# Kernel tuning notes

Measured on AMD Instinct MI355X. Metric: run time of the kernel, lower is better.

Reference implementation:

```python
import jax, jax.numpy as jnp
import numpy as np
import math

B, T, D = 2, 2048, 1024
N_EXP, TOP_K = 8, 2
CAP_FACTOR = 1.25  # train_capacity (module in training mode)
MIN_CAP = 4


def _capacity(num_tokens):
    cap = math.floor(TOP_K * CAP_FACTOR * num_tokens / N_EXP)
    cap += cap % 2
    return max(cap, MIN_CAP)


def setup_inputs() -> dict:
    key = jax.random.key(0)
    k1, k2 = jax.random.split(key)
    x = jax.random.normal(k1, (B, T, D), dtype=jnp.float32)
    w_g = jax.random.normal(k2, (N_EXP, D), dtype=jnp.float32) * 0.02
    return {"x": x, "w_g": w_g}


def reference(x, w_g):
    Bx, Tx, Dx = x.shape
    n_tok = Bx * Tx
    cap = _capacity(n_tok)  # static: depends only on shapes

    # router runs in full precision (router_use_full_prec=True)
    logits = jnp.einsum('btd,ed->bte', x.astype(jnp.float32), w_g.astype(jnp.float32))
    logits = logits.reshape(n_tok, N_EXP)

    top_v, top_i = jax.lax.top_k(logits, TOP_K)          # [n_tok, k]
    # softmax over (-inf)-masked logits == softmax over the k selected logits
    probs_k = jax.nn.softmax(top_v, axis=-1)             # [n_tok, k]

    # expert one-hot mask, ordered [k, tokens, n_exp] (matches torch permute)
    exp_mask = jax.nn.one_hot(top_i, N_EXP, dtype=jnp.int32)   # [n_tok, k, n_exp]
    exp_mask = jnp.transpose(exp_mask, (1, 0, 2))              # [k, n_tok, n_exp]

    # position-in-expert-queue rank via cumsum over flattened (k*tokens)
    rank = jnp.cumsum(exp_mask.reshape(TOP_K * n_tok, N_EXP), axis=0) - 1
    rank = rank.reshape(TOP_K, n_tok, N_EXP)

    exp_mask = exp_mask * (rank < cap).astype(jnp.int32)       # drop overflow tokens
    used_capacity = jnp.sum(exp_mask, axis=(0, 1))             # [n_exp]

    rank_sel = jnp.sum(exp_mask * rank, axis=-1)               # [k, n_tok] int
    keep = jnp.sum(exp_mask, axis=-1).astype(jnp.float32)      # [k, n_tok] 0/1
    w_sel = probs_k.T * keep                                   # [k, n_tok]

    # combine weights: scatter instead of the O(k*tok*n_exp*cap) outer product
    cb_weight = jnp.zeros((n_tok, N_EXP, cap), dtype=jnp.float32)
    tok_ids = jnp.arange(n_tok)
    for k in range(TOP_K):  # tiny static loop over top_k
        cb_weight = cb_weight.at[tok_ids, top_i[:, k], rank_sel[k]].add(w_sel[k])

    sec_mask = cb_weight != 0
    return used_capacity, cb_weight, sec_mask
```

## Files before the change

kernel.cpp:

```cpp
#include <hip/hip_runtime.h>

#define N_TOK   4096
#define DDIM    1024
#define N_EXP   8
#define CAP     1280
#define ROW     (N_EXP * CAP)
#define CB_ELEMS (N_TOK * ROW)

typedef __attribute__((ext_vector_type(4))) float f32x4;


__global__ __launch_bounds__(256) void router_kernel(
    const float* __restrict__ x, const float* __restrict__ wg,
    unsigned int* __restrict__ pk,
    float* __restrict__ p0, float* __restrict__ p1)
{
    __shared__ int se0[4], se1[4];
    const int wave = threadIdx.x >> 6;
    const int lane = threadIdx.x & 63;
    const int t = blockIdx.x * 4 + wave;

    const float4* xt  = (const float4*)(x + (size_t)t * DDIM);
    const float4* wg4 = (const float4*)wg;

    float acc[N_EXP];
#pragma unroll
    for (int e = 0; e < N_EXP; ++e) acc[e] = 0.f;

#pragma unroll
    for (int it = 0; it < 4; ++it) {
        const int d4 = lane + it * 64;
        const float4 xv = xt[d4];
#pragma unroll
        for (int e = 0; e < N_EXP; ++e) {
            const float4 wv = wg4[e * 256 + d4];
            acc[e] = fmaf(xv.x, wv.x,
                     fmaf(xv.y, wv.y,
                     fmaf(xv.z, wv.z,
                     fmaf(xv.w, wv.w, acc[e]))));
        }
    }

#pragma unroll
    for (int e = 0; e < N_EXP; ++e) {
#pragma unroll
        for (int off = 32; off >= 1; off >>= 1)
            acc[e] += __shfl_xor(acc[e], off, 64);
    }

    if (lane == 0) {
        float v0 = -3.402823466e38f, v1 = -3.402823466e38f;
        int   i0 = 0, i1 = 0;
#pragma unroll
        for (int e = 0; e < N_EXP; ++e) {
            const float v = acc[e];
            if (v > v0)      { v1 = v0; i1 = i0; v0 = v; i0 = e; }
            else if (v > v1) { v1 = v;  i1 = e; }
        }
        const float ex  = expf(v1 - v0);
        const float inv = 1.f / (1.f + ex);
        p0[t] = inv;
        p1[t] = ex * inv;
        se0[wave] = i0;
        se1[wave] = i1;
    }
    __syncthreads();

    if (threadIdx.x == 0) {
        const int b = blockIdx.x;
        unsigned short* pks = (unsigned short*)pk;
        const unsigned short h0 = (unsigned short)(se0[0] | (se0[1] << 4) |
                                                   (se0[2] << 8) | (se0[3] << 12));
        const unsigned short h1 = (unsigned short)(se1[0] | (se1[1] << 4) |
                                                   (se1[2] << 8) | (se1[3] << 12));
        pks[b]        = h0;
        pks[1024 + b] = h1;
    }
}

__global__ __launch_bounds__(256) void fill_kernel(
    const unsigned int* __restrict__ pk, const float* __restrict__ p0,
    const float* __restrict__ p1, float* __restrict__ out)
{
    __shared__ int s_e[4], s_r[4];

    const int  b     = blockIdx.x;
    const bool is_cb = (b < 2048);
    const int  t0    = (is_cb ? b : (b - 2048)) * 2;

    const int wave = threadIdx.x >> 6;
    const int lane = threadIdx.x & 63;
    const int tt   = t0 + (wave >> 1);
    const int i    = (wave & 1) * N_TOK + tt;

    unsigned int w[16];
#pragma unroll
    for (int j = 0; j < 16; ++j) w[j] = pk[lane + j * 64];
    const unsigned int wi = pk[i >> 3];

    float* base = out + 8 + (is_cb ? 0 : (size_t)CB_ELEMS) + (size_t)t0 * ROW;
    f32x4* b4   = (f32x4*)base;
    const f32x4 z = {0.f, 0.f, 0.f, 0.f};
#pragma unroll
    for (int it = 0; it < 20; ++it)
        b4[threadIdx.x + it * 256] = z;

    const int e = (int)((wi >> ((i & 7) * 4)) & 0xF);
    int cnt = 0;
#pragma unroll
    for (int j = 0; j < 16; ++j) {
        const int bi = (lane + j * 64) * 8;
#pragma unroll
        for (int s = 0; s < 8; ++s)
            cnt += (bi + s < i && (int)((w[j] >> (4 * s)) & 0xF) == e) ? 1 : 0;
    }
#pragma unroll
    for (int off = 32; off >= 1; off >>= 1)
        cnt += __shfl_xor(cnt, off, 64);
    if (lane == 0) { s_e[wave] = e; s_r[wave] = cnt; }

    __syncthreads();

    if (threadIdx.x < 4) {
        const int r = s_r[threadIdx.x];
        if (r < CAP) {
            const int   t2 = t0 + (threadIdx.x >> 1);
            const float wv = (threadIdx.x & 1) ? p1[t2] : p0[t2];
            const float v  = is_cb ? wv : ((wv != 0.f) ? 1.f : 0.f);
            base[(size_t)(t2 - t0) * ROW + s_e[threadIdx.x] * CAP + r] = v;
        }
    }

    if (b == 0) {
#pragma unroll
        for (int q = 0; q < 2; ++q) {
            const int ee = wave * 2 + q;
            int c = 0;
#pragma unroll
            for (int j = 0; j < 16; ++j) {
#pragma unroll
                for (int s = 0; s < 8; ++s)
                    c += ((int)((w[j] >> (4 * s)) & 0xF) == ee) ? 1 : 0;
            }
#pragma unroll
            for (int off = 32; off >= 1; off >>= 1)
                c += __shfl_xor(c, off, 64);
            if (lane == 0) out[ee] = (float)min(c, CAP);
        }
    }
}

extern "C" void kernel_launch(void* const* d_in, const int* in_sizes, int n_in,
                              void* d_out, int out_size, void* d_ws, size_t ws_size,
                              hipStream_t stream)
{
    const float* x  = (const float*)d_in[0];
    const float* wg = (const float*)d_in[1];
    float* out = (float*)d_out;

    char*         ws = (char*)d_ws;
    unsigned int* pk = (unsigned int*)(ws);
    float*        p0 = (float*)(ws + 4096);
    float*        p1 = (float*)(ws + 20480);

    router_kernel<<<N_TOK / 4, 256, 0, stream>>>(x, wg, pk, p0, p1);
    fill_kernel<<<4096, 256, 0, stream>>>(pk, p0, p1, out);
}
```

Measured before the change: 78.20 us.

## Process sixteen tokens per 1024-thread fill block with packed expert ids staged in LDS

Restructures the fill kernel from 4096 blocks of 256 threads, each handling two tokens, to 512 blocks of 1024 threads, each handling sixteen tokens. The packed top-k expert table is loaded once into shared memory and every wave reads it from there instead of from global memory. One wave now computes the ranks for both top-k slots of its token. The aim is to cut per-block overhead and redundant global reads of the expert table. Each block now zeroes a larger contiguous chunk, which reduces the block count and could lower memory-level parallelism or tail balance.

```diff
diff --git a/kernel.cpp b/kernel.cpp
--- a/kernel.cpp
+++ b/kernel.cpp
@@ -6,6 +6,13 @@
 #define CAP     1280
 #define ROW     (N_EXP * CAP)
 #define CB_ELEMS (N_TOK * ROW)
+
+#define FBLK        512
+#define FTHR        1024
+#define CHUNK_F32   163840
+#define CHUNK4      (CHUNK_F32 / 4)
+#define FITERS      (CHUNK4 / FTHR)
+#define TOK_PER_BLK 16
 
 typedef __attribute__((ext_vector_type(4))) float f32x4;
 
@@ -78,74 +85,77 @@
     }
 }
 
-__global__ __launch_bounds__(256) void fill_kernel(
+__global__ __launch_bounds__(1024) void fill_kernel(
     const unsigned int* __restrict__ pk, const float* __restrict__ p0,
     const float* __restrict__ p1, float* __restrict__ out)
 {
-    __shared__ int s_e[4], s_r[4];
+    __shared__ unsigned int spk[1024];
+    __shared__ int s_e[32], s_r[32];
 
     const int  b     = blockIdx.x;
-    const bool is_cb = (b < 2048);
-    const int  t0    = (is_cb ? b : (b - 2048)) * 2;
+    const bool is_cb = (b < FBLK / 2);
+    const int  tbase = (is_cb ? b : (b - FBLK / 2)) * TOK_PER_BLK;
+
+    spk[threadIdx.x] = pk[threadIdx.x];
+    __syncthreads();
+
+    float* base = out + 8 + (size_t)b * CHUNK_F32;
+    f32x4* b4   = (f32x4*)base;
+    const f32x4 z = {0.f, 0.f, 0.f, 0.f};
+#pragma unroll
+    for (int it = 0; it < FITERS; ++it)
+        b4[threadIdx.x + it * FTHR] = z;
 
     const int wave = threadIdx.x >> 6;
     const int lane = threadIdx.x & 63;
-    const int tt   = t0 + (wave >> 1);
-    const int i    = (wave & 1) * N_TOK + tt;
+    const int tt   = tbase + wave;
 
     unsigned int w[16];
 #pragma unroll
-    for (int j = 0; j < 16; ++j) w[j] = pk[lane + j * 64];
-    const unsigned int wi = pk[i >> 3];
+    for (int j = 0; j < 16; ++j) w[j] = spk[lane + j * 64];
 
-    float* base = out + 8 + (is_cb ? 0 : (size_t)CB_ELEMS) + (size_t)t0 * ROW;
-    f32x4* b4   = (f32x4*)base;
-    const f32x4 z = {0.f, 0.f, 0.f, 0.f};
 #pragma unroll
-    for (int it = 0; it < 20; ++it)
-        b4[threadIdx.x + it * 256] = z;
+    for (int k = 0; k < 2; ++k) {
+        const int i = k * N_TOK + tt;
+        const int e = (int)((spk[i >> 3] >> ((i & 7) * 4)) & 0xF);
+        int cnt = 0;
+#pragma unroll
+        for (int j = 0; j < 16; ++j) {
+            const int bi = (lane + j * 64) * 8;
+#pragma unroll
+            for (int s = 0; s < 8; ++s)
+                cnt += (bi + s < i && (int)((w[j] >> (4 * s)) & 0xF) == e) ? 1 : 0;
+        }
+#pragma unroll
+        for (int off = 32; off >= 1; off >>= 1)
+            cnt += __shfl_xor(cnt, off, 64);
+        if (lane == 0) { s_e[wave * 2 + k] = e; s_r[wave * 2 + k] = cnt; }
+    }
 
-    const int e = (int)((wi >> ((i & 7) * 4)) & 0xF);
-    int cnt = 0;
+    if (b == 0 && wave < N_EXP) {
+        int c = 0;
 #pragma unroll
-    for (int j = 0; j < 16; ++j) {
-        const int bi = (lane + j * 64) * 8;
+        for (int j = 0; j < 16; ++j) {
 #pragma unroll
-        for (int s = 0; s < 8; ++s)
-            cnt += (bi + s < i && (int)((w[j] >> (4 * s)) & 0xF) == e) ? 1 : 0;
+            for (int s = 0; s < 8; ++s)
+                c += ((int)((w[j] >> (4 * s)) & 0xF) == wave) ? 1 : 0;
+        }
+#pragma unroll
+        for (int off = 32; off >= 1; off >>= 1)
+            c += __shfl_xor(c, off, 64);
+        if (lane == 0) out[wave] = (float)min(c, CAP);
     }
-#pragma unroll
-    for (int off = 32; off >= 1; off >>= 1)
-        cnt += __shfl_xor(cnt, off, 64);
-    if (lane == 0) { s_e[wave] = e; s_r[wave] = cnt; }
 
     __syncthreads();
 
-    if (threadIdx.x < 4) {
+    if (threadIdx.x < 32) {
         const int r = s_r[threadIdx.x];
         if (r < CAP) {
-            const int   t2 = t0 + (threadIdx.x >> 1);
+            const int   t2 = tbase + (threadIdx.x >> 1);
             const float wv = (threadIdx.x & 1) ? p1[t2] : p0[t2];
             const float v  = is_cb ? wv : ((wv != 0.f) ? 1.f : 0.f);
-            base[(size_t)(t2 - t0) * ROW + s_e[threadIdx.x] * CAP + r] = v;
-        }
-    }
-
-    if (b == 0) {
-#pragma unroll
-        for (int q = 0; q < 2; ++q) {
-            const int ee = wave * 2 + q;
-            int c = 0;
-#pragma unroll
-            for (int j = 0; j < 16; ++j) {
-#pragma unroll
-                for (int s = 0; s < 8; ++s)
-                    c += ((int)((w[j] >> (4 * s)) & 0xF) == ee) ? 1 : 0;
-            }
-#pragma unroll
-            for (int off = 32; off >= 1; off >>= 1)
-                c += __shfl_xor(c, off, 64);
-            if (lane == 0) out[ee] = (float)min(c, CAP);
+            base[(size_t)(threadIdx.x >> 1) * ROW
+                 + (size_t)s_e[threadIdx.x] * CAP + r] = v;
         }
     }
 }
@@ -164,5 +174,5 @@
     float*        p1 = (float*)(ws + 20480);
 
     router_kernel<<<N_TOK / 4, 256, 0, stream>>>(x, wg, pk, p0, p1);
-    fill_kernel<<<4096, 256, 0, stream>>>(pk, p0, p1, out);
+    fill_kernel<<<FBLK, FTHR, 0, stream>>>(pk, p0, p1, out);
 }
```

After: 219.7 us. +181.0%, slower.

## Align fill blocks to 16B chunks and stage packed expert ids in LDS

Applied to the files above, without the earlier changes.

Each fill block now zeroes a contiguous, 16-byte-aligned chunk of the output, replacing the per-token rows that were offset by the 8-element used_capacity header. This keeps the f32x4 zero stores aligned. Each block computes ranks for the tokens whose nonzero entries can land in its chunk, including neighbouring and edge tokens, and writes a value only if it falls inside its own range. The packed expert ids are first staged in shared memory. In exchange, each block does about twice the rank-counting work and the boundary bookkeeping becomes more complex.

```diff
diff --git a/kernel.cpp b/kernel.cpp
--- a/kernel.cpp
+++ b/kernel.cpp
@@ -6,6 +6,7 @@
 #define CAP     1280
 #define ROW     (N_EXP * CAP)
 #define CB_ELEMS (N_TOK * ROW)
+#define CHUNK   20480
 
 typedef __attribute__((ext_vector_type(4))) float f32x4;
 
@@ -82,72 +83,101 @@
     const unsigned int* __restrict__ pk, const float* __restrict__ p0,
     const float* __restrict__ p1, float* __restrict__ out)
 {
-    __shared__ int s_e[4], s_r[4];
+    __shared__ unsigned int spk[1024];
+    __shared__ int s_e[8], s_r[8], s_used[8];
 
-    const int  b     = blockIdx.x;
-    const bool is_cb = (b < 2048);
-    const int  t0    = (is_cb ? b : (b - 2048)) * 2;
+    const int b  = blockIdx.x;
+    const int lo = b * CHUNK;
 
-    const int wave = threadIdx.x >> 6;
-    const int lane = threadIdx.x & 63;
-    const int tt   = t0 + (wave >> 1);
-    const int i    = (wave & 1) * N_TOK + tt;
-
-    unsigned int w[16];
-#pragma unroll
-    for (int j = 0; j < 16; ++j) w[j] = pk[lane + j * 64];
-    const unsigned int wi = pk[i >> 3];
-
-    float* base = out + 8 + (is_cb ? 0 : (size_t)CB_ELEMS) + (size_t)t0 * ROW;
-    f32x4* b4   = (f32x4*)base;
+    f32x4* b4 = (f32x4*)out + (size_t)b * (CHUNK / 4);
     const f32x4 z = {0.f, 0.f, 0.f, 0.f};
 #pragma unroll
     for (int it = 0; it < 20; ++it)
         b4[threadIdx.x + it * 256] = z;
+    if (b == 4095 && threadIdx.x < 2)
+        ((f32x4*)out)[(size_t)4096 * (CHUNK / 4) + threadIdx.x] = z;
 
-    const int e = (int)((wi >> ((i & 7) * 4)) & 0xF);
-    int cnt = 0;
 #pragma unroll
-    for (int j = 0; j < 16; ++j) {
-        const int bi = (lane + j * 64) * 8;
-#pragma unroll
-        for (int s = 0; s < 8; ++s)
-            cnt += (bi + s < i && (int)((w[j] >> (4 * s)) & 0xF) == e) ? 1 : 0;
-    }
-#pragma unroll
-    for (int off = 32; off >= 1; off >>= 1)
-        cnt += __shfl_xor(cnt, off, 64);
-    if (lane == 0) { s_e[wave] = e; s_r[wave] = cnt; }
-
+    for (int j = 0; j < 4; ++j)
+        spk[threadIdx.x + j * 256] = pk[threadIdx.x + j * 256];
     __syncthreads();
 
-    if (threadIdx.x < 4) {
-        const int r = s_r[threadIdx.x];
-        if (r < CAP) {
-            const int   t2 = t0 + (threadIdx.x >> 1);
-            const float wv = (threadIdx.x & 1) ? p1[t2] : p0[t2];
-            const float v  = is_cb ? wv : ((wv != 0.f) ? 1.f : 0.f);
-            base[(size_t)(t2 - t0) * ROW + s_e[threadIdx.x] * CAP + r] = v;
+    const int wave = threadIdx.x >> 6;
+    const int lane = threadIdx.x & 63;
+    const int c    = b & 2047;
+    const int t0   = 2 * c;
+    const int tc   = (wave == 0) ? t0 - 1 : (wave == 1) ? t0 :
+                     (wave == 2) ? t0 + 1 : ((b == 2048) ? N_TOK - 1 : -1);
+
+    unsigned int w[16];
+#pragma unroll
+    for (int j = 0; j < 16; ++j) w[j] = spk[lane + j * 64];
+
+    if (tc >= 0 && tc < N_TOK) {
+#pragma unroll
+        for (int k = 0; k < 2; ++k) {
+            const int i = k * N_TOK + tc;
+            const int e = (int)((spk[i >> 3] >> ((i & 7) * 4)) & 0xF);
+            int cnt = 0;
+#pragma unroll
+            for (int j = 0; j < 16; ++j) {
+                const int bi = (lane + j * 64) * 8;
+#pragma unroll
+                for (int s = 0; s < 8; ++s)
+                    cnt += (bi + s < i &&
+                            (int)((w[j] >> (4 * s)) & 0xF) == e) ? 1 : 0;
+            }
+#pragma unroll
+            for (int off = 32; off >= 1; off >>= 1)
+                cnt += __shfl_xor(cnt, off, 64);
+            if (lane == 0) { s_e[wave * 2 + k] = e; s_r[wave * 2 + k] = cnt; }
         }
+    } else if (lane == 0) {
+        s_r[wave * 2] = 1 << 20; s_r[wave * 2 + 1] = 1 << 20;
+        s_e[wave * 2] = 0;       s_e[wave * 2 + 1] = 0;
     }
 
     if (b == 0) {
 #pragma unroll
         for (int q = 0; q < 2; ++q) {
             const int ee = wave * 2 + q;
-            int c = 0;
+            int cu = 0;
 #pragma unroll
             for (int j = 0; j < 16; ++j) {
 #pragma unroll
                 for (int s = 0; s < 8; ++s)
-                    c += ((int)((w[j] >> (4 * s)) & 0xF) == ee) ? 1 : 0;
+                    cu += ((int)((w[j] >> (4 * s)) & 0xF) == ee) ? 1 : 0;
             }
 #pragma unroll
             for (int off = 32; off >= 1; off >>= 1)
-                c += __shfl_xor(c, off, 64);
-            if (lane == 0) out[ee] = (float)min(c, CAP);
+                cu += __shfl_xor(cu, off, 64);
+            if (lane == 0) s_used[ee] = min(cu, CAP);
         }
     }
+
+    __syncthreads();
+
+    if (threadIdx.x < 16) {
+        const int  q  = threadIdx.x >> 1;
+        const bool mk = threadIdx.x & 1;
+        const int  r  = s_r[q];
+        if (r < CAP) {
+            const int wv2 = q >> 1;
+            const int k   = q & 1;
+            const int tt  = (wv2 == 0) ? t0 - 1 : (wv2 == 1) ? t0 :
+                            (wv2 == 2) ? t0 + 1 : N_TOK - 1;
+            const int g   = 8 + tt * ROW + s_e[q] * CAP + r
+                            + (mk ? CB_ELEMS : 0);
+            const int hi  = lo + CHUNK + ((b == 4095) ? 8 : 0);
+            if (g >= lo && g < hi) {
+                const float wv = k ? p1[tt] : p0[tt];
+                out[(size_t)g] = mk ? ((wv != 0.f) ? 1.f : 0.f) : wv;
+            }
+        }
+    }
+
+    if (b == 0 && threadIdx.x < 8)
+        out[threadIdx.x] = (float)s_used[threadIdx.x];
 }
 
 extern "C" void kernel_launch(void* const* d_in, const int* in_sizes, int n_in,
```

New measurement: 120.5 us. +54.1%, slower.

## Split fill into grid-stride zero kernel and separate sparse fixup kernel

Applied to the files above, without the earlier changes.

The combined zero-and-scatter kernel becomes two kernels. A 256-block grid-stride kernel zeroes the whole output buffer with vector stores, then a fixup kernel stages the packed expert indices in shared memory, computes the rank for each (k, token) pair, and writes the cb weight and sec mask entries. The intent is to make the large zero-fill a plain streaming write, decoupled from the rank computation. In exchange it adds an extra kernel launch and a dependency between the zero and scatter passes.

```diff
diff --git a/kernel.cpp b/kernel.cpp
--- a/kernel.cpp
+++ b/kernel.cpp
@@ -78,34 +78,42 @@
     }
 }
 
-__global__ __launch_bounds__(256) void fill_kernel(
+__global__ __launch_bounds__(256) void zero_kernel(float* __restrict__ out)
+{
+    f32x4* dst = (f32x4*)out;
+    const int gid = blockIdx.x * 256 + threadIdx.x;
+    const f32x4 z = {0.f, 0.f, 0.f, 0.f};
+    size_t i = gid;
+#pragma unroll 8
+    for (int it = 0; it < 320; ++it) {
+        dst[i] = z;
+        i += 65536;
+    }
+    if (gid < 2)
+        dst[(size_t)320 * 65536 + gid] = z;
+}
+
+__global__ __launch_bounds__(256) void fixup_kernel(
     const unsigned int* __restrict__ pk, const float* __restrict__ p0,
     const float* __restrict__ p1, float* __restrict__ out)
 {
-    __shared__ int s_e[4], s_r[4];
-
-    const int  b     = blockIdx.x;
-    const bool is_cb = (b < 2048);
-    const int  t0    = (is_cb ? b : (b - 2048)) * 2;
+    __shared__ unsigned int spk[1024];
+#pragma unroll
+    for (int j = 0; j < 4; ++j)
+        spk[threadIdx.x + j * 256] = pk[threadIdx.x + j * 256];
+    __syncthreads();
 
     const int wave = threadIdx.x >> 6;
     const int lane = threadIdx.x & 63;
-    const int tt   = t0 + (wave >> 1);
-    const int i    = (wave & 1) * N_TOK + tt;
+    const int i    = blockIdx.x * 4 + wave;
+    const int t    = i & (N_TOK - 1);
+    const int k    = i >> 12;
 
     unsigned int w[16];
 #pragma unroll
-    for (int j = 0; j < 16; ++j) w[j] = pk[lane + j * 64];
-    const unsigned int wi = pk[i >> 3];
+    for (int j = 0; j < 16; ++j) w[j] = spk[lane + j * 64];
 
-    float* base = out + 8 + (is_cb ? 0 : (size_t)CB_ELEMS) + (size_t)t0 * ROW;
-    f32x4* b4   = (f32x4*)base;
-    const f32x4 z = {0.f, 0.f, 0.f, 0.f};
-#pragma unroll
-    for (int it = 0; it < 20; ++it)
-        b4[threadIdx.x + it * 256] = z;
-
-    const int e = (int)((wi >> ((i & 7) * 4)) & 0xF);
+    const int e = (int)((spk[i >> 3] >> ((i & 7) * 4)) & 0xF);
     int cnt = 0;
 #pragma unroll
     for (int j = 0; j < 16; ++j) {
@@ -117,21 +125,15 @@
 #pragma unroll
     for (int off = 32; off >= 1; off >>= 1)
         cnt += __shfl_xor(cnt, off, 64);
-    if (lane == 0) { s_e[wave] = e; s_r[wave] = cnt; }
 
-    __syncthreads();
-
-    if (threadIdx.x < 4) {
-        const int r = s_r[threadIdx.x];
-        if (r < CAP) {
-            const int   t2 = t0 + (threadIdx.x >> 1);
-            const float wv = (threadIdx.x & 1) ? p1[t2] : p0[t2];
-            const float v  = is_cb ? wv : ((wv != 0.f) ? 1.f : 0.f);
-            base[(size_t)(t2 - t0) * ROW + s_e[threadIdx.x] * CAP + r] = v;
-        }
+    if (lane == 0 && cnt < CAP) {
+        const float wv = k ? p1[t] : p0[t];
+        float* cb = out + 8 + (size_t)t * ROW + (size_t)e * CAP + cnt;
+        cb[0]        = wv;
+        cb[CB_ELEMS] = (wv != 0.f) ? 1.f : 0.f;
     }
 
-    if (b == 0) {
+    if (blockIdx.x == 0) {
 #pragma unroll
         for (int q = 0; q < 2; ++q) {
             const int ee = wave * 2 + q;
@@ -164,5 +166,6 @@
     float*        p1 = (float*)(ws + 20480);
 
     router_kernel<<<N_TOK / 4, 256, 0, stream>>>(x, wg, pk, p0, p1);
-    fill_kernel<<<4096, 256, 0, stream>>>(pk, p0, p1, out);
+    zero_kernel<<<256, 256, 0, stream>>>(out);
+    fixup_kernel<<<2048, 256, 0, stream>>>(pk, p0, p1, out);
 }
```

Result: slower. 82.90 us (+6.0%).
